# Kernel optimization log

Hardware: AMD Instinct MI355X
Metric: run time of the kernel (lower is better)

The kernel has to match this reference:

```python
import jax, jax.numpy as jnp
import numpy as np

WS = 4        # window_size
HEADS = 12    # num_heads


def setup_inputs() -> dict:
    key = jax.random.key(0)
    k1, k2, k3 = jax.random.split(key, 3)
    B, N, E = 32, 4096, 384
    x = jax.random.normal(k1, (B, N, E), dtype=jnp.float32)
    w_in = jax.random.normal(k2, (3 * E, E), dtype=jnp.float32) * 0.02
    b_in = jnp.zeros((3 * E,), dtype=jnp.float32)
    w_out = jax.random.normal(k3, (E, E), dtype=jnp.float32) * 0.02
    b_out = jnp.zeros((E,), dtype=jnp.float32)
    return {"x": x, "w_in": w_in, "b_in": b_in, "w_out": w_out, "b_out": b_out}


def reference(x, w_in, b_in, w_out, b_out):
    B, N, E = x.shape
    H = W = int(np.sqrt(N))
    nh, nw = H // WS, W // WS
    hd = E // HEADS
    T = WS * WS  # tokens per window

    # window partition: [B, H, W, E] -> [B*nh*nw, T, E]
    xw = x.reshape(B, nh, WS, nw, WS, E)
    xw = xw.transpose(0, 1, 3, 2, 4, 5).reshape(-1, T, E)

    # packed QKV projection (torch nn.MultiheadAttention in_proj)
    qkv = xw @ w_in.T + b_in                      # [nWin, T, 3E]
    q, k, v = jnp.split(qkv, 3, axis=-1)          # each [nWin, T, E]

    def split_heads(t):
        return t.reshape(-1, T, HEADS, hd).transpose(0, 2, 1, 3)  # [nWin, h, T, hd]

    q, k, v = split_heads(q), split_heads(k), split_heads(v)
    scale = 1.0 / np.sqrt(hd).astype(np.float32)
    scores = jnp.einsum('whqd,whkd->whqk', q * scale, k)          # [nWin, h, T, T]
    attn = jax.nn.softmax(scores, axis=-1)
    out = jnp.einsum('whqk,whkd->whqd', attn, v)                  # [nWin, h, T, hd]
    out = out.transpose(0, 2, 1, 3).reshape(-1, T, E)
    out = out @ w_out.T + b_out                                   # out_proj

    # window reverse: [B*nh*nw, T, E] -> [B, N, E]
    out = out.reshape(B, nh, nw, WS, WS, E)
    out = out.transpose(0, 1, 3, 2, 4, 5).reshape(B, N, E)
    return out
```

## Files before the change

kernel.cpp:

```cpp
#include <hip/hip_runtime.h>
#include <hip/hip_bf16.h>

typedef __attribute__((ext_vector_type(8))) short short8;
typedef __attribute__((ext_vector_type(4))) float f32x4;

static __device__ __forceinline__ f32x4 MFMA16(short8 a, short8 b, f32x4 c) {
    return __builtin_amdgcn_mfma_f32_16x16x32_bf16(a, b, c, 0, 0, 0);
}
static __device__ __forceinline__ unsigned short f2bf(float f) {
    union { __hip_bfloat16 h; unsigned short u; } c;
    c.h = __float2bfloat16(f);
    return c.u;
}
static __device__ __forceinline__ void gload16(const void* g, void* l) {
    __builtin_amdgcn_global_load_lds(
        (const __attribute__((address_space(1))) unsigned int*)g,
        (__attribute__((address_space(3))) unsigned int*)l, 16, 0, 0);
}

constexpr size_t kWstOff = 0;
constexpr size_t kWosOff = 884736;
constexpr size_t kBrrOff = 1179648;
constexpr size_t kAttOff = 1184256;

__global__ void prep(const float* __restrict__ w_in, const float* __restrict__ b_in,
                     const float* __restrict__ w_out,
                     char* __restrict__ wst, char* __restrict__ wos,
                     float* __restrict__ brr)
{
    const int i = blockIdx.x * 256 + threadIdx.x;
    if (i < 55296) {
        int hp = i / 9216, rem = i % 9216;
        int s = rem / 1536, slot16 = rem % 1536;
        int row = slot16 >> 3, sl = slot16 & 7;
        int c8 = sl ^ (row & 7);
        int hh = row / 96, rr = row % 96;
        int sec = rr >> 5, d = rr & 31;
        int srow = sec * 384 + (hp * 2 + hh) * 32 + d;
        int k0 = s * 64 + c8 * 8;
        const float4* src = (const float4*)(w_in + (size_t)srow * 384 + k0);
        float4 a = src[0], b = src[1];
        uint4 w;
        w.x = f2bf(a.x) | ((unsigned)f2bf(a.y) << 16);
        w.y = f2bf(a.z) | ((unsigned)f2bf(a.w) << 16);
        w.z = f2bf(b.x) | ((unsigned)f2bf(b.y) << 16);
        w.w = f2bf(b.z) | ((unsigned)f2bf(b.w) << 16);
        *(uint4*)(wst + (size_t)i * 16) = w;
    } else {
        int j = i - 55296;
        int nb = j / 6144, rem = j % 6144;
        int s = rem / 1024, slot16 = rem % 1024;
        int row = slot16 >> 3, sl = slot16 & 7;
        int c8 = sl ^ (row & 7);
        int srow = nb * 128 + row;
        int k0 = s * 64 + c8 * 8;
        const float4* src = (const float4*)(w_out + (size_t)srow * 384 + k0);
        float4 a = src[0], b = src[1];
        uint4 w;
        w.x = f2bf(a.x) | ((unsigned)f2bf(a.y) << 16);
        w.y = f2bf(a.z) | ((unsigned)f2bf(a.w) << 16);
        w.z = f2bf(b.x) | ((unsigned)f2bf(b.y) << 16);
        w.w = f2bf(b.z) | ((unsigned)f2bf(b.w) << 16);
        *(uint4*)(wos + (size_t)j * 16) = w;
    }
    if (i < 1152) {
        int h = i / 96, jj = i % 96;
        int sec = jj >> 5, d = jj & 31;
        brr[i] = b_in[sec * 384 + h * 32 + d];
    }
}

__global__ __launch_bounds__(512, 2)
void qkv_attn(const float* __restrict__ x, const char* __restrict__ wst,
              const float* __restrict__ brr, char* __restrict__ attst)
{
    __shared__ __align__(16) char smem[81920];

    const int tid  = threadIdx.x;
    const int lane = tid & 63, wid = tid >> 6;
    const int g = lane >> 4, r16 = lane & 15;
    const int wm = wid >> 1, wn = wid & 1;

    int b = blockIdx.x;
    int L = (b & 7) * 768 + (b >> 3);
    const int mblk = L / 6, hp = L - mblk * 6;
    const int head = hp * 2 + wn;

    const int arow = tid >> 2, aq = tid & 3;
    int T0 = mblk * 128 + arow;
    int win0 = T0 >> 4, t4 = T0 & 15;
    int bb0 = win0 >> 8, wh = (win0 >> 4) & 15, ww = win0 & 15;
    const float* xrow = x + ((size_t)bb0 * 4096 +
                             (size_t)((wh * 4 + (t4 >> 2)) * 64 + ww * 4 + (t4 & 3))) * 384
                          + aq * 16;

    float4 af[4];
    auto load_A = [&](int s) {
        const float4* xp = (const float4*)(xrow + s * 64);
        #pragma unroll
        for (int j = 0; j < 4; ++j) af[j] = xp[j];
    };
    auto write_A = [&](int buf) {
        #pragma unroll
        for (int j = 0; j < 2; ++j) {
            uint4 w;
            w.x = f2bf(af[2*j].x)   | ((unsigned)f2bf(af[2*j].y)   << 16);
            w.y = f2bf(af[2*j].z)   | ((unsigned)f2bf(af[2*j].w)   << 16);
            w.z = f2bf(af[2*j+1].x) | ((unsigned)f2bf(af[2*j+1].y) << 16);
            w.w = f2bf(af[2*j+1].z) | ((unsigned)f2bf(af[2*j+1].w) << 16);
            int slot = (aq * 2 + j) ^ (arow & 7);
            *(uint4*)(smem + buf * 16384 + arow * 128 + slot * 16) = w;
        }
    };
    const char* wst_blk = wst + (size_t)hp * 147456;
    auto stage_B = [&](int s, int buf) {
        char* dst = smem + 32768 + buf * 24576 + tid * 16;
        const char* src = wst_blk + s * 24576 + tid * 16;
        #pragma unroll
        for (int j = 0; j < 3; ++j) gload16(src + j * 8192, dst + j * 8192);
    };

    f32x4 acc[2][6] = {};
    auto compute = [&](int buf) {
        const char* ab = smem + buf * 16384;
        const char* bbp = smem + 32768 + buf * 24576;
        #pragma unroll
        for (int c = 0; c < 2; ++c) {
            const int sw = ((c * 4 + g) ^ (r16 & 7)) << 4;
            short8 a[2], bf[6];
            #pragma unroll
            for (int mi = 0; mi < 2; ++mi)
                a[mi] = *(const short8*)(ab + (wm * 32 + mi * 16 + r16) * 128 + sw);
            #pragma unroll
            for (int ni = 0; ni < 6; ++ni)
                bf[ni] = *(const short8*)(bbp + (wn * 96 + ni * 16 + r16) * 128 + sw);
            #pragma unroll
            for (int mi = 0; mi < 2; ++mi)
                #pragma unroll
                for (int ni = 0; ni < 6; ++ni)
                    acc[mi][ni] = MFMA16(a[mi], bf[ni], acc[mi][ni]);
        }
    };

    load_A(0);
    stage_B(0, 0);
    write_A(0);
    for (int s = 0; s < 6; ++s) {
        __syncthreads();
        if (s < 5) { load_A(s + 1); stage_B(s + 1, (s + 1) & 1); }
        compute(s & 1);
        if (s < 5) write_A((s + 1) & 1);
    }
    __syncthreads();

    float bias[6];
    #pragma unroll
    for (int ni = 0; ni < 6; ++ni) bias[ni] = brr[head * 96 + ni * 16 + r16];

    #pragma unroll
    for (int mi = 0; mi < 2; ++mi) {
        const int win = wm * 2 + mi;
        #pragma unroll
        for (int ni = 0; ni < 6; ++ni) {
            const int sec = ni >> 1;
            const int d = (ni & 1) * 16 + r16;
            float v0 = acc[mi][ni][0] + bias[ni];
            float v1 = acc[mi][ni][1] + bias[ni];
            float v2 = acc[mi][ni][2] + bias[ni];
            float v3 = acc[mi][ni][3] + bias[ni];
            uint2 w;
            w.x = f2bf(v0) | ((unsigned)f2bf(v1) << 16);
            w.y = f2bf(v2) | ((unsigned)f2bf(v3) << 16);
            *(uint2*)(smem + win * 6144 + wn * 3072 + sec * 1024 + d * 32 + g * 8) = w;
        }
    }

    const float kC = 0.17677669529663687f * 1.4426950408889634f;
    const f32x4 zero = {0.f, 0.f, 0.f, 0.f};

    #pragma unroll
    for (int i = 0; i < 2; ++i) {
        const int win = wm * 2 + i;
        const char* base = smem + win * 6144 + wn * 3072;

        union U8 { unsigned short e[8]; short8 v; };
        U8 ku, qu;
        #pragma unroll
        for (int j = 0; j < 8; ++j) {
            const int off = (g * 8 + j) * 32 + r16 * 2;
            qu.e[j] = *(const unsigned short*)(base + off);
            ku.e[j] = *(const unsigned short*)(base + 1024 + off);
        }
        f32x4 s = MFMA16(ku.v, qu.v, zero);

        float m = fmaxf(fmaxf(s[0], s[1]), fmaxf(s[2], s[3]));
        m = fmaxf(m, __shfl_xor(m, 16, 64));
        m = fmaxf(m, __shfl_xor(m, 32, 64));
        float p[4], sum = 0.f;
        #pragma unroll
        for (int r = 0; r < 4; ++r) { p[r] = exp2f((s[r] - m) * kC); sum += p[r]; }
        sum += __shfl_xor(sum, 16, 64);
        sum += __shfl_xor(sum, 32, 64);
        const float inv = 1.f / sum;

        U8 pu;
        pu.e[0] = f2bf(p[0] * inv); pu.e[1] = f2bf(p[1] * inv);
        pu.e[2] = f2bf(p[2] * inv); pu.e[3] = f2bf(p[3] * inv);
        pu.e[4] = 0; pu.e[5] = 0; pu.e[6] = 0; pu.e[7] = 0;

        f32x4 o[2];
        #pragma unroll
        for (int ti = 0; ti < 2; ++ti) {
            U8 vu;
            *(uint2*)&vu.e[0] = *(const uint2*)(base + 2048 + (ti * 16 + r16) * 32 + g * 8);
            vu.e[4] = 0; vu.e[5] = 0; vu.e[6] = 0; vu.e[7] = 0;
            o[ti] = MFMA16(pu.v, vu.v, zero);
        }
        #pragma unroll
        for (int ti = 0; ti < 2; ++ti) {
            #pragma unroll
            for (int r = 0; r < 4; ++r) {
                int row7 = win * 16 + g * 4 + r;
                int col = head * 32 + ti * 16 + r16;
                int sst = col >> 6;
                int sl = ((col >> 3) & 7) ^ (row7 & 7);
                *(unsigned short*)(attst + (size_t)mblk * 98304 + sst * 16384
                                   + row7 * 128 + sl * 16 + (col & 7) * 2)
                    = f2bf(o[ti][r]);
            }
        }
    }
}

__global__ __launch_bounds__(256, 2)
void out_proj(const char* __restrict__ attst, const char* __restrict__ wos,
              const float* __restrict__ b_out, float* __restrict__ out)
{
    __shared__ __align__(16) char smem[65536];

    const int tid  = threadIdx.x;
    const int lane = tid & 63, wid = tid >> 6;
    const int g = lane >> 4, r16 = lane & 15;
    const int wm = wid >> 1, wn = wid & 1;

    int b = blockIdx.x;
    int L = (b & 7) * 384 + (b >> 3);
    const int mblk = L / 3, nblk = L - mblk * 3;

    auto stage = [&](int s, int buf) {
        const char* asrc = attst + (size_t)mblk * 98304 + s * 16384 + wid * 4096 + lane * 16;
        const char* bsrc = wos   + (size_t)nblk * 98304 + s * 16384 + wid * 4096 + lane * 16;
        char* adst = smem + buf * 16384 + wid * 4096;
        char* bdst = smem + 32768 + buf * 16384 + wid * 4096;
        #pragma unroll
        for (int j = 0; j < 4; ++j) {
            gload16(asrc + j * 1024, adst + j * 1024);
            gload16(bsrc + j * 1024, bdst + j * 1024);
        }
    };

    f32x4 acc[4][4] = {};
    auto compute = [&](int buf) {
        const char* ab = smem + buf * 16384;
        const char* bbp = smem + 32768 + buf * 16384;
        #pragma unroll
        for (int c = 0; c < 2; ++c) {
            const int sw = ((c * 4 + g) ^ (r16 & 7)) << 4;
            short8 a[4], bf[4];
            #pragma unroll
            for (int mi = 0; mi < 4; ++mi)
                a[mi] = *(const short8*)(ab + (wm * 64 + mi * 16 + r16) * 128 + sw);
            #pragma unroll
            for (int ni = 0; ni < 4; ++ni)
                bf[ni] = *(const short8*)(bbp + (wn * 64 + ni * 16 + r16) * 128 + sw);
            #pragma unroll
            for (int mi = 0; mi < 4; ++mi)
                #pragma unroll
                for (int ni = 0; ni < 4; ++ni)
                    acc[mi][ni] = MFMA16(a[mi], bf[ni], acc[mi][ni]);
        }
    };

    stage(0, 0);
    for (int s = 0; s < 6; ++s) {
        __syncthreads();
        if (s < 5) stage(s + 1, (s + 1) & 1);
        compute(s & 1);
    }

    float bias[4];
    #pragma unroll
    for (int ni = 0; ni < 4; ++ni) bias[ni] = b_out[nblk * 128 + wn * 64 + ni * 16 + r16];

    #pragma unroll
    for (int mi = 0; mi < 4; ++mi) {
        #pragma unroll
        for (int r = 0; r < 4; ++r) {
            int T = mblk * 128 + wm * 64 + mi * 16 + g * 4 + r;
            int win = T >> 4, tt = T & 15;
            int bb = win >> 8, wh = (win >> 4) & 15, ww = win & 15;
            size_t o = ((size_t)bb * 4096 + (wh * 4 + (tt >> 2)) * 64 + ww * 4 + (tt & 3)) * 384
                     + nblk * 128 + wn * 64;
            #pragma unroll
            for (int ni = 0; ni < 4; ++ni)
                out[o + ni * 16 + r16] = acc[mi][ni][r] + bias[ni];
        }
    }
}

extern "C" void kernel_launch(void* const* d_in, const int* in_sizes, int n_in,
                              void* d_out, int out_size, void* d_ws, size_t ws_size,
                              hipStream_t stream) {
    const float* x     = (const float*)d_in[0];
    const float* w_in  = (const float*)d_in[1];
    const float* b_in  = (const float*)d_in[2];
    const float* w_out = (const float*)d_in[3];
    const float* b_out = (const float*)d_in[4];
    float* out = (float*)d_out;

    char* ws = (char*)d_ws;
    char*  wst = ws + kWstOff;
    char*  wos = ws + kWosOff;
    float* brr = (float*)(ws + kBrrOff);
    char*  att = ws + kAttOff;

    prep<<<dim3(288), dim3(256), 0, stream>>>(w_in, b_in, w_out, wst, wos, brr);
    qkv_attn<<<dim3(6144), dim3(512), 0, stream>>>(x, wst, brr, att);
    out_proj<<<dim3(3072), dim3(256), 0, stream>>>(att, wos, b_out, out);
}
```

Measured before the change: 286.6 us.

## Load A fragments directly from global into registers, drop A LDS staging

The x activation tile is no longer staged through shared memory. Each wave now loads its MFMA A-fragment rows straight from global memory and converts them to bf16 in registers, so LDS shrinks to the double-buffered weight tiles and launch bounds allow more resident blocks. This removes the LDS write/read round-trip for A and raises occupancy. In exchange, the two waves that share each row tile (wn=0 and wn=1) both load it from global, the global loads are no longer prefetched ahead of compute, and the per-lane access pattern is less coalesced.

Result: slower. 479.8 us (+67.4%).

```diff
diff --git a/kernel.cpp b/kernel.cpp
--- a/kernel.cpp
+++ b/kernel.cpp
@@ -70,11 +70,11 @@
     }
 }
 
-__global__ __launch_bounds__(512, 2)
+__global__ __launch_bounds__(512, 6)
 void qkv_attn(const float* __restrict__ x, const char* __restrict__ wst,
               const float* __restrict__ brr, char* __restrict__ attst)
 {
-    __shared__ __align__(16) char smem[81920];
+    __shared__ __align__(16) char smem[49152];
 
     const int tid  = threadIdx.x;
     const int lane = tid & 63, wid = tid >> 6;
@@ -86,70 +86,55 @@
     const int mblk = L / 6, hp = L - mblk * 6;
     const int head = hp * 2 + wn;
 
-    const int arow = tid >> 2, aq = tid & 3;
-    int T0 = mblk * 128 + arow;
-    int win0 = T0 >> 4, t4 = T0 & 15;
-    int bb0 = win0 >> 8, wh = (win0 >> 4) & 15, ww = win0 & 15;
-    const float* xrow = x + ((size_t)bb0 * 4096 +
-                             (size_t)((wh * 4 + (t4 >> 2)) * 64 + ww * 4 + (t4 & 3))) * 384
-                          + aq * 16;
-
-    float4 af[4];
-    auto load_A = [&](int s) {
-        const float4* xp = (const float4*)(xrow + s * 64);
-        #pragma unroll
-        for (int j = 0; j < 4; ++j) af[j] = xp[j];
-    };
-    auto write_A = [&](int buf) {
-        #pragma unroll
-        for (int j = 0; j < 2; ++j) {
-            uint4 w;
-            w.x = f2bf(af[2*j].x)   | ((unsigned)f2bf(af[2*j].y)   << 16);
-            w.y = f2bf(af[2*j].z)   | ((unsigned)f2bf(af[2*j].w)   << 16);
-            w.z = f2bf(af[2*j+1].x) | ((unsigned)f2bf(af[2*j+1].y) << 16);
-            w.w = f2bf(af[2*j+1].z) | ((unsigned)f2bf(af[2*j+1].w) << 16);
-            int slot = (aq * 2 + j) ^ (arow & 7);
-            *(uint4*)(smem + buf * 16384 + arow * 128 + slot * 16) = w;
-        }
-    };
+    const float* arow[2];
+    #pragma unroll
+    for (int mi = 0; mi < 2; ++mi) {
+        int T = mblk * 128 + wm * 32 + mi * 16 + r16;
+        int win0 = T >> 4, t4 = T & 15;
+        int bb0 = win0 >> 8, wh = (win0 >> 4) & 15, ww = win0 & 15;
+        arow[mi] = x + ((size_t)bb0 * 4096 +
+                        (size_t)((wh * 4 + (t4 >> 2)) * 64 + ww * 4 + (t4 & 3))) * 384
+                     + g * 8;
+    }
+
     const char* wst_blk = wst + (size_t)hp * 147456;
     auto stage_B = [&](int s, int buf) {
-        char* dst = smem + 32768 + buf * 24576 + tid * 16;
+        char* dst = smem + buf * 24576 + tid * 16;
         const char* src = wst_blk + s * 24576 + tid * 16;
         #pragma unroll
         for (int j = 0; j < 3; ++j) gload16(src + j * 8192, dst + j * 8192);
     };
 
     f32x4 acc[2][6] = {};
-    auto compute = [&](int buf) {
-        const char* ab = smem + buf * 16384;
-        const char* bbp = smem + 32768 + buf * 24576;
+    auto compute = [&](int s, int buf) {
+        const char* bbp = smem + buf * 24576;
         #pragma unroll
         for (int c = 0; c < 2; ++c) {
             const int sw = ((c * 4 + g) ^ (r16 & 7)) << 4;
-            short8 a[2], bf[6];
-            #pragma unroll
-            for (int mi = 0; mi < 2; ++mi)
-                a[mi] = *(const short8*)(ab + (wm * 32 + mi * 16 + r16) * 128 + sw);
-            #pragma unroll
-            for (int ni = 0; ni < 6; ++ni)
-                bf[ni] = *(const short8*)(bbp + (wn * 96 + ni * 16 + r16) * 128 + sw);
-            #pragma unroll
-            for (int mi = 0; mi < 2; ++mi)
-                #pragma unroll
-                for (int ni = 0; ni < 6; ++ni)
-                    acc[mi][ni] = MFMA16(a[mi], bf[ni], acc[mi][ni]);
+            union U8 { unsigned u[4]; short8 v; } a[2];
+            #pragma unroll
+            for (int mi = 0; mi < 2; ++mi) {
+                const float4* ap = (const float4*)(arow[mi] + s * 64 + c * 32);
+                float4 lo = ap[0], hi = ap[1];
+                a[mi].u[0] = f2bf(lo.x) | ((unsigned)f2bf(lo.y) << 16);
+                a[mi].u[1] = f2bf(lo.z) | ((unsigned)f2bf(lo.w) << 16);
+                a[mi].u[2] = f2bf(hi.x) | ((unsigned)f2bf(hi.y) << 16);
+                a[mi].u[3] = f2bf(hi.z) | ((unsigned)f2bf(hi.w) << 16);
+            }
+            #pragma unroll
+            for (int ni = 0; ni < 6; ++ni) {
+                short8 bf = *(const short8*)(bbp + (wn * 96 + ni * 16 + r16) * 128 + sw);
+                acc[0][ni] = MFMA16(a[0].v, bf, acc[0][ni]);
+                acc[1][ni] = MFMA16(a[1].v, bf, acc[1][ni]);
+            }
         }
     };
 
-    load_A(0);
     stage_B(0, 0);
-    write_A(0);
     for (int s = 0; s < 6; ++s) {
         __syncthreads();
-        if (s < 5) { load_A(s + 1); stage_B(s + 1, (s + 1) & 1); }
-        compute(s & 1);
-        if (s < 5) write_A((s + 1) & 1);
+        if (s < 5) stage_B(s + 1, (s + 1) & 1);
+        compute(s, s & 1);
     }
     __syncthreads();
 
```

## Single-buffer QKV GEMM LDS to raise occupancy to four blocks per CU

Applied to the files above, without the earlier changes.

Drops the double-buffered LDS staging for the A (x) and B (weight) tiles in the fused QKV+attention kernel, cutting the declared shared memory from 80 KB to 48 KB and raising the launch-bounds occupancy hint from 2 to 4 blocks. The B tile stage now happens after an extra barrier, once compute on the current buffer is done. This gives up within-block overlap of global-to-LDS loads with MFMA work and adds a barrier per k-step. In return it relies on more resident blocks to hide latency, and the tighter register budget may cause spills. The later attention part may also need LDS beyond 48 KB, which is not visible here.

After: 283.2 us. About the same (-1.2%).

```diff
diff --git a/kernel.cpp b/kernel.cpp
--- a/kernel.cpp
+++ b/kernel.cpp
@@ -70,11 +70,11 @@
     }
 }
 
-__global__ __launch_bounds__(512, 2)
+__global__ __launch_bounds__(512, 4)
 void qkv_attn(const float* __restrict__ x, const char* __restrict__ wst,
               const float* __restrict__ brr, char* __restrict__ attst)
 {
-    __shared__ __align__(16) char smem[81920];
+    __shared__ __align__(16) char smem[49152];
 
     const int tid  = threadIdx.x;
     const int lane = tid & 63, wid = tid >> 6;
@@ -100,7 +100,7 @@
         #pragma unroll
         for (int j = 0; j < 4; ++j) af[j] = xp[j];
     };
-    auto write_A = [&](int buf) {
+    auto write_A = [&]() {
         #pragma unroll
         for (int j = 0; j < 2; ++j) {
             uint4 w;
@@ -109,31 +109,29 @@
             w.z = f2bf(af[2*j+1].x) | ((unsigned)f2bf(af[2*j+1].y) << 16);
             w.w = f2bf(af[2*j+1].z) | ((unsigned)f2bf(af[2*j+1].w) << 16);
             int slot = (aq * 2 + j) ^ (arow & 7);
-            *(uint4*)(smem + buf * 16384 + arow * 128 + slot * 16) = w;
+            *(uint4*)(smem + arow * 128 + slot * 16) = w;
         }
     };
     const char* wst_blk = wst + (size_t)hp * 147456;
-    auto stage_B = [&](int s, int buf) {
-        char* dst = smem + 32768 + buf * 24576 + tid * 16;
+    auto stage_B = [&](int s) {
+        char* dst = smem + 16384 + tid * 16;
         const char* src = wst_blk + s * 24576 + tid * 16;
         #pragma unroll
         for (int j = 0; j < 3; ++j) gload16(src + j * 8192, dst + j * 8192);
     };
 
     f32x4 acc[2][6] = {};
-    auto compute = [&](int buf) {
-        const char* ab = smem + buf * 16384;
-        const char* bbp = smem + 32768 + buf * 24576;
+    auto compute = [&]() {
         #pragma unroll
         for (int c = 0; c < 2; ++c) {
             const int sw = ((c * 4 + g) ^ (r16 & 7)) << 4;
             short8 a[2], bf[6];
             #pragma unroll
             for (int mi = 0; mi < 2; ++mi)
-                a[mi] = *(const short8*)(ab + (wm * 32 + mi * 16 + r16) * 128 + sw);
+                a[mi] = *(const short8*)(smem + (wm * 32 + mi * 16 + r16) * 128 + sw);
             #pragma unroll
             for (int ni = 0; ni < 6; ++ni)
-                bf[ni] = *(const short8*)(bbp + (wn * 96 + ni * 16 + r16) * 128 + sw);
+                bf[ni] = *(const short8*)(smem + 16384 + (wn * 96 + ni * 16 + r16) * 128 + sw);
             #pragma unroll
             for (int mi = 0; mi < 2; ++mi)
                 #pragma unroll
@@ -143,13 +141,17 @@
     };
 
     load_A(0);
-    stage_B(0, 0);
-    write_A(0);
+    stage_B(0);
+    write_A();
     for (int s = 0; s < 6; ++s) {
         __syncthreads();
-        if (s < 5) { load_A(s + 1); stage_B(s + 1, (s + 1) & 1); }
-        compute(s & 1);
-        if (s < 5) write_A((s + 1) & 1);
+        if (s < 5) load_A(s + 1);
+        compute();
+        if (s < 5) {
+            __syncthreads();
+            stage_B(s + 1);
+            write_A();
+        }
     }
     __syncthreads();
 
```
